# Kernel tuning notes

Hardware: AMD Instinct MI355X
Metric: run time of the kernel (lower is better)

The kernel has to match this reference:

```python
import jax, jax.numpy as jnp
import numpy as np

B, T, C = 4, 2048, 1024
H, HS = 16, 64


def setup_inputs() -> dict:
    key = jax.random.key(0)
    ks = jax.random.split(key, 5)
    scale = (H * C) ** (-0.5)
    x = jax.random.normal(ks[0], (B, T, C), dtype=jnp.float32)
    Wk = jax.random.normal(ks[1], (H, C, HS), dtype=jnp.float32) * scale
    Wq = jax.random.normal(ks[2], (H, C, HS), dtype=jnp.float32) * scale
    Wv = jax.random.normal(ks[3], (H, C, HS), dtype=jnp.float32) * scale
    proj_w = jax.random.normal(ks[4], (C, C), dtype=jnp.float32) / C ** 0.5
    proj_b = jnp.zeros((C,), dtype=jnp.float32)
    return {"x": x, "Wk": Wk, "Wq": Wq, "Wv": Wv, "proj_w": proj_w, "proj_b": proj_b}


def reference(x, Wk, Wq, Wv, proj_w, proj_b):
    b, t, c = x.shape
    # per-head projections: (B,T,C) x (H,C,D) -> (B,H,T,D)
    q = jnp.einsum('btc,hcd->bhtd', x, Wq)
    k = jnp.einsum('btc,hcd->bhtd', x, Wk)
    v = jnp.einsum('btc,hcd->bhtd', x, Wv)
    # NOTE: original module does not scale by 1/sqrt(head_size)
    wei = jnp.einsum('bhtd,bhsd->bhts', q, k)  # (B,H,T,T)
    causal = jnp.tril(jnp.ones((t, t), dtype=bool))
    wei = jnp.where(causal, wei, -jnp.inf)
    wei = jax.nn.softmax(wei, axis=-1)
    out = jnp.einsum('bhts,bhsd->bhtd', wei, v)
    out = out.transpose(0, 2, 1, 3).reshape(b, t, c)  # concat heads
    return out @ proj_w + proj_b
```

## Files before the change

### kernel.cpp

```cpp
#include <hip/hip_runtime.h>

typedef unsigned short u16;
typedef u16 u16x4 __attribute__((ext_vector_type(4)));
typedef u16 u16x8 __attribute__((ext_vector_type(8)));
typedef unsigned u32x2 __attribute__((ext_vector_type(2)));
typedef __bf16 bf16x8 __attribute__((ext_vector_type(8)));
typedef float f32x4 __attribute__((ext_vector_type(4)));

#define DEV static __device__ __forceinline__

DEV u16 f2bf(float f) {
  union { float f; unsigned u; } v; v.f = f;
  return (u16)((v.u + 0x7FFFu + ((v.u >> 16) & 1u)) >> 16);
}

DEV unsigned pack2(float a, float b) {
  unsigned ua = __builtin_bit_cast(unsigned, a) + 0x8000u;
  unsigned ub = __builtin_bit_cast(unsigned, b) + 0x8000u;
  return (ua >> 16) | (ub & 0xFFFF0000u);
}

DEV void async16(const void* g, void* l) {
  __builtin_amdgcn_global_load_lds((const __attribute__((address_space(1))) void*)g,
                                   (__attribute__((address_space(3))) void*)l, 16, 0, 0);
}

DEV f32x4 mfma16(bf16x8 a, bf16x8 b, f32x4 c) {
  return __builtin_amdgcn_mfma_f32_16x16x32_bf16(a, b, c, 0, 0, 0);
}

DEV float exp2fast(float x) { return __builtin_amdgcn_exp2f(x); }

__global__ __launch_bounds__(256) void k_pack_x(const float* __restrict__ x,
                                                u16* __restrict__ o) {
  int i = (blockIdx.x * 256 + threadIdx.x) * 4;
  float4 v = *(const float4*)(x + i);
  u16x4 t = { f2bf(v.x), f2bf(v.y), f2bf(v.z), f2bf(v.w) };
  *(u16x4*)(o + i) = t;
}

__global__ __launch_bounds__(256) void k_tpack(const float* __restrict__ src,
                                               u16* __restrict__ dst,
                                               int rows, int cols, float scale) {
  __shared__ float t[64 * 72];
  const int tid = threadIdx.x;
  src += (size_t)blockIdx.z * rows * cols;
  dst += (size_t)blockIdx.z * rows * cols;
  const int c0 = blockIdx.x * 64, r0 = blockIdx.y * 64;
  const int rr = tid >> 2, cb = (tid & 3) * 16;
  const float* s = src + (size_t)(r0 + rr) * cols + c0 + cb;
  float4 v0 = *(const float4*)(s + 0);
  float4 v1 = *(const float4*)(s + 4);
  float4 v2 = *(const float4*)(s + 8);
  float4 v3 = *(const float4*)(s + 12);
  *(float4*)(t + rr * 72 + cb + 0)  = v0;
  *(float4*)(t + rr * 72 + cb + 4)  = v1;
  *(float4*)(t + rr * 72 + cb + 8)  = v2;
  *(float4*)(t + rr * 72 + cb + 12) = v3;
  __syncthreads();
  const int dd = tid >> 2, eb = (tid & 3) * 16;
  u16x8 o0, o1;
#pragma unroll
  for (int e = 0; e < 8; ++e) o0[e] = f2bf(t[(eb + e) * 72 + dd] * scale);
#pragma unroll
  for (int e = 0; e < 8; ++e) o1[e] = f2bf(t[(eb + 8 + e) * 72 + dd] * scale);
  u16* dp = dst + (size_t)(c0 + dd) * rows + r0 + eb;
  *(u16x8*)dp = o0;
  *(u16x8*)(dp + 8) = o1;
}

template <int MODE>
__global__ __launch_bounds__(256) void k_gemm(const u16* __restrict__ A,
                                              const u16* __restrict__ Bt,
                                              u16* __restrict__ qd,
                                              u16* __restrict__ kd,
                                              u16* __restrict__ vd,
                                              float* __restrict__ out,
                                              const float* __restrict__ bias) {
  __shared__ u16 As[128 * 64];
  __shared__ u16 Bs[128 * 64];
  const int tid = threadIdx.x;
  const int wave = tid >> 6, lane = tid & 63;
  const int quad = lane >> 4, l15 = lane & 15;
  const int wm = wave & 1, wn = wave >> 1;
  const size_t mb = blockIdx.y, nb = blockIdx.x;

  const int lrow = lane >> 3;
  const int lchunk = ((lane & 7) ^ lrow) << 3;
  const u16* ga = A + (mb * 128 + wave * 32 + lrow) * 1024 + lchunk;
  const u16* gb = Bt + (nb * 128 + wave * 32 + lrow) * 1024 + lchunk;
  u16* adst = As + wave * 2048;
  u16* bdst = Bs + wave * 2048;

  const int sa0 = ((0 + quad) ^ (l15 & 7)) << 3;
  const int sa1 = ((4 + quad) ^ (l15 & 7)) << 3;

  f32x4 acc[4][4] = {};
  for (int k0 = 0; k0 < 1024; k0 += 64) {
#pragma unroll
    for (int m = 0; m < 4; ++m) {
      async16(ga + m * 8 * 1024, adst + m * 512);
      async16(gb + m * 8 * 1024, bdst + m * 512);
    }
    ga += 64; gb += 64;
    __syncthreads();
#pragma unroll
    for (int c = 0; c < 2; ++c) {
      const int swz = c ? sa1 : sa0;
      bf16x8 af[4], bf[4];
#pragma unroll
      for (int i = 0; i < 4; ++i)
        af[i] = *(const bf16x8*)(As + (wm * 64 + i * 16 + l15) * 64 + swz);
#pragma unroll
      for (int j = 0; j < 4; ++j)
        bf[j] = *(const bf16x8*)(Bs + (wn * 64 + j * 16 + l15) * 64 + swz);
#pragma unroll
      for (int i = 0; i < 4; ++i)
#pragma unroll
        for (int j = 0; j < 4; ++j)
          acc[i][j] = mfma16(af[i], bf[j], acc[i][j]);
    }
    __syncthreads();
  }

  const size_t m0 = mb * 128 + wm * 64;
  const int n0 = (int)nb * 128 + wn * 64;
  if (MODE == 0) {
#pragma unroll
    for (int j = 0; j < 4; ++j) {
      const int n = n0 + j * 16 + l15;
      const int p = n >> 10, hh = (n >> 6) & 15, d = n & 63;
      if (p == 2) {
#pragma unroll
        for (int i = 0; i < 4; ++i) {
          const size_t m = m0 + i * 16 + quad * 4;
          const size_t bb = m >> 11, tt = m & 2047;
          u16x4 pk = { f2bf(acc[i][j][0]), f2bf(acc[i][j][1]),
                       f2bf(acc[i][j][2]), f2bf(acc[i][j][3]) };
          *(u16x4*)(vd + ((bb * 16 + hh) * 64 + d) * 2048 + tt) = pk;
        }
      } else {
        u16* dst = (p == 0) ? qd : kd;
#pragma unroll
        for (int i = 0; i < 4; ++i)
#pragma unroll
          for (int r = 0; r < 4; ++r) {
            const size_t m = m0 + i * 16 + quad * 4 + r;
            const size_t bb = m >> 11, tt = m & 2047;
            dst[((bb * 16 + hh) * 2048 + tt) * 64 + d] = f2bf(acc[i][j][r]);
          }
      }
    }
  } else {
#pragma unroll
    for (int j = 0; j < 4; ++j) {
      const int n = n0 + j * 16 + l15;
      const float bv = bias[n];
#pragma unroll
      for (int i = 0; i < 4; ++i)
#pragma unroll
        for (int r = 0; r < 4; ++r) {
          const size_t m = m0 + i * 16 + quad * 4 + r;
          out[m * 1024 + n] = acc[i][j][r] + bv;
        }
    }
  }
}

__global__ __launch_bounds__(256) void k_attn(const u16* __restrict__ Qg,
                                              const u16* __restrict__ Kg,
                                              const u16* __restrict__ Vtg,
                                              u16* __restrict__ Og) {
  __shared__ u16 Kbuf[2 * 4096];
  __shared__ u16 Vbuf[2 * 4096];
  __shared__ u16 Pbuf[4 * 32 * 72];
  const int tid = threadIdx.x;
  const int wave = tid >> 6, lane = tid & 63;
  const int quad = lane >> 4, l15 = lane & 15;
  const int quad4 = quad * 4, quad8 = quad * 8;
  const int bh = blockIdx.x;
  const int qb = 15 - (int)blockIdx.y;
  const u16* kg = Kg + (size_t)bh * 2048 * 64;
  const u16* vg = Vtg + (size_t)bh * 64 * 2048;
  u16* Pw = Pbuf + wave * (32 * 72);
  const int b = bh >> 4, h = bh & 15;

  const int lrow = lane >> 3;
  const int lchunk = ((lane & 7) ^ lrow) << 3;
  const u16* kst = kg + (size_t)(wave * 16 + lrow) * 64 + lchunk;
  const u16* vst = vg + (size_t)(wave * 16 + lrow) * 2048 + lchunk;
  u16* kdst0 = Kbuf + wave * 1024;
  u16* vdst0 = Vbuf + wave * 1024;

  const int rowoff = l15 * 64;
  const int swz0 = ((0 + quad) ^ (l15 & 7)) << 3;
  const int swz1 = ((4 + quad) ^ (l15 & 7)) << 3;

  const int qlo = qb * 128 + wave * 32;
  const int ntw = 2 * qb + 1 + (wave >> 1);
  const int ntb = 2 * qb + 2;
  const u16* qg = Qg + ((size_t)bh * 2048 + (size_t)qb * 128) * 64;

  bf16x8 qf[2][2];
#pragma unroll
  for (int i = 0; i < 2; ++i)
#pragma unroll
    for (int c = 0; c < 2; ++c)
      qf[i][c] = *(const bf16x8*)(qg + (size_t)(wave * 32 + i * 16 + l15) * 64 +
                                  c * 32 + quad8);

  f32x4 oacc[2][4] = {};
  float lsum[2] = {0.f, 0.f};
  const f32x4 fzero = {};

  async16(kst, kdst0);
  async16(kst + 512, kdst0 + 512);
  async16(vst, vdst0);
  async16(vst + 16384, vdst0 + 512);

  for (int it = 0; it < ntb; ++it) {
    __syncthreads();

    if (it + 1 < ntb) {
      const int buf = (it + 1) & 1;
      const size_t s0n = (size_t)(it + 1) * 64;
      async16(kst + s0n * 64,       kdst0 + buf * 4096);
      async16(kst + s0n * 64 + 512, kdst0 + buf * 4096 + 512);
      async16(vst + s0n,            vdst0 + buf * 4096);
      async16(vst + s0n + 16384,    vdst0 + buf * 4096 + 512);
    }

    if (it < ntw) {
      const int s0 = it * 64;
      const u16* Kb = Kbuf + (it & 1) * 4096;
      const u16* Vb = Vbuf + (it & 1) * 4096;

      f32x4 sacc[4][2];
#pragma unroll
      for (int j = 0; j < 4; ++j) {
        bf16x8 kf0 = *(const bf16x8*)(Kb + j * 1024 + rowoff + swz0);
        bf16x8 kf1 = *(const bf16x8*)(Kb + j * 1024 + rowoff + swz1);
        sacc[j][0] = mfma16(kf0, qf[0][0], fzero);
        sacc[j][0] = mfma16(kf1, qf[0][1], sacc[j][0]);
        sacc[j][1] = mfma16(kf0, qf[1][0], fzero);
        sacc[j][1] = mfma16(kf1, qf[1][1], sacc[j][1]);
      }

#pragma unroll
      for (int j = 0; j < 4; ++j)
#pragma unroll
        for (int i = 0; i < 2; ++i)
#pragma unroll
          for (int r = 0; r < 4; ++r)
            sacc[j][i][r] = exp2fast(sacc[j][i][r]);

      if (it == ntw - 1) {
#pragma unroll
        for (int j = 0; j < 4; ++j)
#pragma unroll
          for (int i = 0; i < 2; ++i)
#pragma unroll
            for (int r = 0; r < 4; ++r)
              if (s0 + j * 16 + quad4 + r > qlo + i * 16 + l15) sacc[j][i][r] = 0.f;
      }

#pragma unroll
      for (int j = 0; j < 4; ++j)
#pragma unroll
        for (int i = 0; i < 2; ++i) {
          lsum[i] += (sacc[j][i][0] + sacc[j][i][1]) +
                     (sacc[j][i][2] + sacc[j][i][3]);
          u32x2 pk = { pack2(sacc[j][i][0], sacc[j][i][1]),
                       pack2(sacc[j][i][2], sacc[j][i][3]) };
          *(u32x2*)(Pw + (i * 16 + l15) * 72 + j * 16 + quad4) = pk;
        }

      bf16x8 pa[2][2];
#pragma unroll
      for (int i = 0; i < 2; ++i)
#pragma unroll
        for (int c = 0; c < 2; ++c)
          pa[i][c] = *(const bf16x8*)(Pw + (i * 16 + l15) * 72 + c * 32 + quad8);

#pragma unroll
      for (int n = 0; n < 4; ++n) {
        bf16x8 vf0 = *(const bf16x8*)(Vb + n * 1024 + rowoff + swz0);
        bf16x8 vf1 = *(const bf16x8*)(Vb + n * 1024 + rowoff + swz1);
        oacc[0][n] = mfma16(pa[0][0], vf0, oacc[0][n]);
        oacc[0][n] = mfma16(pa[0][1], vf1, oacc[0][n]);
        oacc[1][n] = mfma16(pa[1][0], vf0, oacc[1][n]);
        oacc[1][n] = mfma16(pa[1][1], vf1, oacc[1][n]);
      }
    }
  }

#pragma unroll
  for (int i = 0; i < 2; ++i) {
    lsum[i] += __shfl_xor(lsum[i], 16, 64);
    lsum[i] += __shfl_xor(lsum[i], 32, 64);
  }
#pragma unroll
  for (int i = 0; i < 2; ++i)
#pragma unroll
    for (int r = 0; r < 4; ++r) {
      const float inv = 1.0f / __shfl(lsum[i], quad4 + r, 16);
      const size_t t = (size_t)qb * 128 + wave * 32 + i * 16 + quad4 + r;
#pragma unroll
      for (int n = 0; n < 4; ++n)
        Og[((size_t)b * 2048 + t) * 1024 + h * 64 + n * 16 + l15] =
            f2bf(oacc[i][n][r] * inv);
    }
}

extern "C" void kernel_launch(void* const* d_in, const int* in_sizes, int n_in,
                              void* d_out, int out_size, void* d_ws, size_t ws_size,
                              hipStream_t stream) {
  const float* x  = (const float*)d_in[0];
  const float* Wk = (const float*)d_in[1];
  const float* Wq = (const float*)d_in[2];
  const float* Wv = (const float*)d_in[3];
  const float* pw = (const float*)d_in[4];
  const float* pb = (const float*)d_in[5];
  float* out = (float*)d_out;
  char* ws = (char*)d_ws;

  u16* xb  = (u16*)(ws + 0);
  u16* wT  = (u16*)(ws + 16777216);
  u16* pwT = (u16*)(ws + 23068672);
  u16* q   = (u16*)(ws + 25165824);
  u16* kb  = (u16*)(ws + 41943040);
  u16* vt  = (u16*)(ws + 58720256);
  u16* att = (u16*)(ws + 0);

  const float LOG2E = 1.44269504088896340736f;
  k_pack_x<<<8192, 256, 0, stream>>>(x, xb);
  k_tpack<<<dim3(1, 16, 16), 256, 0, stream>>>(Wq, wT + 0,           1024, 64, LOG2E);
  k_tpack<<<dim3(1, 16, 16), 256, 0, stream>>>(Wk, wT + 1024 * 1024, 1024, 64, 1.0f);
  k_tpack<<<dim3(1, 16, 16), 256, 0, stream>>>(Wv, wT + 2048 * 1024, 1024, 64, 1.0f);
  k_tpack<<<dim3(16, 16, 1), 256, 0, stream>>>(pw, pwT, 1024, 1024, 1.0f);
  k_gemm<0><<<dim3(24, 64), 256, 0, stream>>>(xb, wT, q, kb, vt, nullptr, nullptr);
  k_attn<<<dim3(64, 16), 256, 0, stream>>>(q, kb, vt, att);
  k_gemm<1><<<dim3(8, 64), 256, 0, stream>>>(att, pwT, nullptr, nullptr, nullptr, out, pb);
}
```

Baseline: 255.6 us.

## Fuse prep kernels into one launch and enlarge QKV GEMM M tile

Merges the x bf16 pack and four weight transpose-pack launches into a single k_prep kernel that dispatches on block index, removing four launches and their serialization gaps. Templates the GEMM on the M-tile size and uses a 256x128 tile for the QKV projection, halving the grid and doubling the reuse of each B tile loaded into LDS. The larger tile doubles accumulator registers and LDS for A, which can lower occupancy, and the grid of 768 blocks may fill the CUs less evenly.

```diff
diff --git a/kernel.cpp b/kernel.cpp
--- a/kernel.cpp
+++ b/kernel.cpp
@@ -31,22 +31,42 @@
 
 DEV float exp2fast(float x) { return __builtin_amdgcn_exp2f(x); }
 
-__global__ __launch_bounds__(256) void k_pack_x(const float* __restrict__ x,
-                                                u16* __restrict__ o) {
-  int i = (blockIdx.x * 256 + threadIdx.x) * 4;
-  float4 v = *(const float4*)(x + i);
-  u16x4 t = { f2bf(v.x), f2bf(v.y), f2bf(v.z), f2bf(v.w) };
-  *(u16x4*)(o + i) = t;
-}
-
-__global__ __launch_bounds__(256) void k_tpack(const float* __restrict__ src,
-                                               u16* __restrict__ dst,
-                                               int rows, int cols, float scale) {
+__global__ __launch_bounds__(256) void k_prep(const float* __restrict__ x,
+                                              const float* __restrict__ Wk,
+                                              const float* __restrict__ Wq,
+                                              const float* __restrict__ Wv,
+                                              const float* __restrict__ pw,
+                                              u16* __restrict__ xb,
+                                              u16* __restrict__ wT,
+                                              u16* __restrict__ pwT) {
   __shared__ float t[64 * 72];
-  const int tid = threadIdx.x;
-  src += (size_t)blockIdx.z * rows * cols;
-  dst += (size_t)blockIdx.z * rows * cols;
-  const int c0 = blockIdx.x * 64, r0 = blockIdx.y * 64;
+  const int bid = blockIdx.x, tid = threadIdx.x;
+  if (bid < 8192) {
+    int i = bid * 1024 + tid * 4;
+    float4 v = *(const float4*)(x + i);
+    u16x4 o = { f2bf(v.x), f2bf(v.y), f2bf(v.z), f2bf(v.w) };
+    *(u16x4*)(xb + i) = o;
+    return;
+  }
+  const int role = bid - 8192;
+  const float* src;
+  u16* dst;
+  int rows, cols, bx, by, bz;
+  float scale;
+  if (role < 768) {
+    const int w = role >> 8, rem = role & 255;
+    src = (w == 0) ? Wq : ((w == 1) ? Wk : Wv);
+    dst = wT + (size_t)w * 1024 * 1024;
+    scale = (w == 0) ? 1.44269504088896340736f : 1.0f;
+    rows = 1024; cols = 64; bx = 0; by = rem >> 4; bz = rem & 15;
+  } else {
+    const int p = role - 768;
+    src = pw; dst = pwT; scale = 1.0f;
+    rows = 1024; cols = 1024; bx = p & 15; by = p >> 4; bz = 0;
+  }
+  src += (size_t)bz * rows * cols;
+  dst += (size_t)bz * rows * cols;
+  const int c0 = bx * 64, r0 = by * 64;
   const int rr = tid >> 2, cb = (tid & 3) * 16;
   const float* s = src + (size_t)(r0 + rr) * cols + c0 + cb;
   float4 v0 = *(const float4*)(s + 0);
@@ -69,7 +89,7 @@
   *(u16x8*)(dp + 8) = o1;
 }
 
-template <int MODE>
+template <int MODE, int NI>
 __global__ __launch_bounds__(256) void k_gemm(const u16* __restrict__ A,
                                               const u16* __restrict__ Bt,
                                               u16* __restrict__ qd,
@@ -77,7 +97,7 @@
                                               u16* __restrict__ vd,
                                               float* __restrict__ out,
                                               const float* __restrict__ bias) {
-  __shared__ u16 As[128 * 64];
+  __shared__ u16 As[NI * 32 * 64];
   __shared__ u16 Bs[128 * 64];
   const int tid = threadIdx.x;
   const int wave = tid >> 6, lane = tid & 63;
@@ -87,35 +107,36 @@
 
   const int lrow = lane >> 3;
   const int lchunk = ((lane & 7) ^ lrow) << 3;
-  const u16* ga = A + (mb * 128 + wave * 32 + lrow) * 1024 + lchunk;
+  const u16* ga = A + (mb * (NI * 32) + wave * (NI * 8) + lrow) * 1024 + lchunk;
   const u16* gb = Bt + (nb * 128 + wave * 32 + lrow) * 1024 + lchunk;
-  u16* adst = As + wave * 2048;
+  u16* adst = As + wave * (NI * 512);
   u16* bdst = Bs + wave * 2048;
 
   const int sa0 = ((0 + quad) ^ (l15 & 7)) << 3;
   const int sa1 = ((4 + quad) ^ (l15 & 7)) << 3;
 
-  f32x4 acc[4][4] = {};
+  f32x4 acc[NI][4] = {};
   for (int k0 = 0; k0 < 1024; k0 += 64) {
 #pragma unroll
-    for (int m = 0; m < 4; ++m) {
+    for (int m = 0; m < NI; ++m)
       async16(ga + m * 8 * 1024, adst + m * 512);
+#pragma unroll
+    for (int m = 0; m < 4; ++m)
       async16(gb + m * 8 * 1024, bdst + m * 512);
-    }
     ga += 64; gb += 64;
     __syncthreads();
 #pragma unroll
     for (int c = 0; c < 2; ++c) {
       const int swz = c ? sa1 : sa0;
-      bf16x8 af[4], bf[4];
-#pragma unroll
-      for (int i = 0; i < 4; ++i)
-        af[i] = *(const bf16x8*)(As + (wm * 64 + i * 16 + l15) * 64 + swz);
+      bf16x8 af[NI], bf[4];
+#pragma unroll
+      for (int i = 0; i < NI; ++i)
+        af[i] = *(const bf16x8*)(As + (wm * (NI * 16) + i * 16 + l15) * 64 + swz);
 #pragma unroll
       for (int j = 0; j < 4; ++j)
         bf[j] = *(const bf16x8*)(Bs + (wn * 64 + j * 16 + l15) * 64 + swz);
 #pragma unroll
-      for (int i = 0; i < 4; ++i)
+      for (int i = 0; i < NI; ++i)
 #pragma unroll
         for (int j = 0; j < 4; ++j)
           acc[i][j] = mfma16(af[i], bf[j], acc[i][j]);
@@ -123,7 +144,7 @@
     __syncthreads();
   }
 
-  const size_t m0 = mb * 128 + wm * 64;
+  const size_t m0 = mb * (NI * 32) + wm * (NI * 16);
   const int n0 = (int)nb * 128 + wn * 64;
   if (MODE == 0) {
 #pragma unroll
@@ -132,7 +153,7 @@
       const int p = n >> 10, hh = (n >> 6) & 15, d = n & 63;
       if (p == 2) {
 #pragma unroll
-        for (int i = 0; i < 4; ++i) {
+        for (int i = 0; i < NI; ++i) {
           const size_t m = m0 + i * 16 + quad * 4;
           const size_t bb = m >> 11, tt = m & 2047;
           u16x4 pk = { f2bf(acc[i][j][0]), f2bf(acc[i][j][1]),
@@ -142,7 +163,7 @@
       } else {
         u16* dst = (p == 0) ? qd : kd;
 #pragma unroll
-        for (int i = 0; i < 4; ++i)
+        for (int i = 0; i < NI; ++i)
 #pragma unroll
           for (int r = 0; r < 4; ++r) {
             const size_t m = m0 + i * 16 + quad * 4 + r;
@@ -157,7 +178,7 @@
       const int n = n0 + j * 16 + l15;
       const float bv = bias[n];
 #pragma unroll
-      for (int i = 0; i < 4; ++i)
+      for (int i = 0; i < NI; ++i)
 #pragma unroll
         for (int r = 0; r < 4; ++r) {
           const size_t m = m0 + i * 16 + quad * 4 + r;
@@ -332,13 +353,8 @@
   u16* vt  = (u16*)(ws + 58720256);
   u16* att = (u16*)(ws + 0);
 
-  const float LOG2E = 1.44269504088896340736f;
-  k_pack_x<<<8192, 256, 0, stream>>>(x, xb);
-  k_tpack<<<dim3(1, 16, 16), 256, 0, stream>>>(Wq, wT + 0,           1024, 64, LOG2E);
-  k_tpack<<<dim3(1, 16, 16), 256, 0, stream>>>(Wk, wT + 1024 * 1024, 1024, 64, 1.0f);
-  k_tpack<<<dim3(1, 16, 16), 256, 0, stream>>>(Wv, wT + 2048 * 1024, 1024, 64, 1.0f);
-  k_tpack<<<dim3(16, 16, 1), 256, 0, stream>>>(pw, pwT, 1024, 1024, 1.0f);
-  k_gemm<0><<<dim3(24, 64), 256, 0, stream>>>(xb, wT, q, kb, vt, nullptr, nullptr);
+  k_prep<<<9216, 256, 0, stream>>>(x, Wk, Wq, Wv, pw, xb, wT, pwT);
+  k_gemm<0, 8><<<dim3(24, 32), 256, 0, stream>>>(xb, wT, q, kb, vt, nullptr, nullptr);
   k_attn<<<dim3(64, 16), 256, 0, stream>>>(q, kb, vt, att);
-  k_gemm<1><<<dim3(8, 64), 256, 0, stream>>>(att, pwT, nullptr, nullptr, nullptr, out, pb);
-}
+  k_gemm<1, 4><<<dim3(8, 64), 256, 0, stream>>>(att, pwT, nullptr, nullptr, nullptr, out, pb);
+}
```

Result: slower. 272.4 us (+6.6%).
